# Kernel optimization log

Measured on AMD Instinct MI355X. Metric: run time of the kernel, lower is better.

The kernel has to match this reference:

```python
import jax, jax.numpy as jnp
import numpy as np

HID = 2048      # hidden_size
H = 16          # num query heads
KV = 4          # num kv heads
HD = HID // H   # head_dim = 128
THETA = 1000000.0
T = 2048        # tokens (single causal sequence)


def _rope(x, positions):
    # neox-style rotate-half RoPE over full head_dim. x: [T, h, HD]
    half = HD // 2
    inv_freq = THETA ** (-jnp.arange(half, dtype=jnp.float32) * 2.0 / HD)  # [half]
    freqs = positions.astype(jnp.float32)[:, None] * inv_freq              # [T, half]
    cos = jnp.cos(freqs)[:, None, :]
    sin = jnp.sin(freqs)[:, None, :]
    x1, x2 = x[..., :half], x[..., half:]
    return jnp.concatenate([x1 * cos - x2 * sin, x2 * cos + x1 * sin], axis=-1)


def setup_inputs() -> dict:
    key = jax.random.key(0)
    k1, k2, k3 = jax.random.split(key, 3)
    hidden_states = jax.random.normal(k1, (T, HID), jnp.float32) * 0.02
    w_qkv = jax.random.normal(k2, (HID, (H + 2 * KV) * HD), jnp.float32) * 0.02
    w_o = jax.random.normal(k3, (H * HD, HID), jnp.float32) * 0.02
    positions = jnp.arange(T, dtype=jnp.int32)
    return {"hidden_states": hidden_states, "w_qkv": w_qkv, "w_o": w_o,
            "positions": positions}


def reference(hidden_states, w_qkv, w_o, positions):
    q_size, kv_size = H * HD, KV * HD
    qkv = hidden_states @ w_qkv                                  # [T, q+2kv]
    q = qkv[:, :q_size].reshape(T, H, HD)
    k = qkv[:, q_size:q_size + kv_size].reshape(T, KV, HD)
    v = qkv[:, q_size + kv_size:].reshape(T, KV, HD)
    q = _rope(q, positions)
    k = _rope(k, positions)
    # GQA: expand kv heads to query heads
    group = H // KV
    k_e = jnp.repeat(k, group, axis=1)                           # [T, H, HD]
    v_e = jnp.repeat(v, group, axis=1)
    scale = HD ** -0.5
    scores = jnp.einsum('thd,shd->hts', q, k_e) * scale          # [H, T, T]
    causal = positions[:, None] >= positions[None, :]            # [T, T]
    scores = jnp.where(causal[None, :, :], scores, -1e30)
    attn = jax.nn.softmax(scores, axis=-1)
    o = jnp.einsum('hts,shd->thd', attn, v_e).reshape(T, H * HD)
    return o @ w_o
```

## Files before the change

### kernel.cpp

```cpp
#include <hip/hip_runtime.h>
#include <hip/hip_bf16.h>

#define T_LEN 2048
#define HID 2048
#define NH 16
#define NKV 4
#define HD 128
#define QKV_COLS 3072

typedef __attribute__((ext_vector_type(8))) short bf16x8;
typedef __attribute__((ext_vector_type(4))) float f32x4;

static __device__ __forceinline__ ushort f2bf(float f) {
  __hip_bfloat16 h = __float2bfloat16(f);
  return *reinterpret_cast<ushort*>(&h);
}
static __device__ __forceinline__ float bf2f(ushort u) {
  union { unsigned int i; float f; } v;
  v.i = ((unsigned int)u) << 16;
  return v.f;
}

static __device__ __forceinline__ void async_copy16(const ushort* g, ushort* l) {
  __builtin_amdgcn_global_load_lds(
      (const __attribute__((address_space(1))) unsigned int*)g,
      (__attribute__((address_space(3))) unsigned int*)l, 16, 0, 0);
}

__global__ __launch_bounds__(256) void cast_f32_bf16(
    const float* __restrict__ x, ushort* __restrict__ y, int n) {
  int idx = (blockIdx.x * 256 + threadIdx.x) * 4;
  if (idx < n) {
    float4 v = *(const float4*)(x + idx);
    ushort4 o;
    o.x = f2bf(v.x); o.y = f2bf(v.y); o.z = f2bf(v.z); o.w = f2bf(v.w);
    *(ushort4*)(y + idx) = o;
  }
}

__global__ __launch_bounds__(256) void transpose_cast(
    const float* __restrict__ W, ushort* __restrict__ WT, int K, int N) {
  __shared__ float t[64][65];
  const int bk = blockIdx.x * 64, bn = blockIdx.y * 64;
  const int tid = threadIdx.x;
  const int c = tid & 63;
#pragma unroll
  for (int i = 0; i < 16; ++i) {
    int r = (tid >> 6) + i * 4;
    t[r][c] = W[(size_t)(bk + r) * N + bn + c];
  }
  __syncthreads();
#pragma unroll
  for (int i = 0; i < 16; ++i) {
    int r = (tid >> 6) + i * 4;
    WT[(size_t)(bn + r) * K + bk + c] = f2bf(t[c][r]);
  }
}

template <bool OUT_BF16>
__global__ __launch_bounds__(256, 4) void gemm_bt(
    const ushort* __restrict__ A, const ushort* __restrict__ BT,
    void* __restrict__ C, int M, int N, int K) {
  __shared__ __align__(16) ushort lds[1536 * 8];
  const int tid = threadIdx.x;
  const int bm = blockIdx.y * 64, bn = blockIdx.x * 128;
  const int wave = tid >> 6, lane = tid & 63;
  const int lr = lane & 15, lq = lane >> 4;
  const int wm = (wave & 1) * 32, wn = (wave >> 1) * 64;

  f32x4 acc[2][4];
#pragma unroll
  for (int i = 0; i < 2; ++i)
#pragma unroll
    for (int j = 0; j < 4; ++j) {
      acc[i][j][0] = 0.f; acc[i][j][1] = 0.f;
      acc[i][j][2] = 0.f; acc[i][j][3] = 0.f;
    }

  for (int k0 = 0; k0 < K; k0 += 64) {
#pragma unroll
    for (int it = 0; it < 2; ++it) {
      int c = it * 256 + tid;
      int row = c >> 3, sl = c & 7, kc = sl ^ (row & 7);
      async_copy16(A + (size_t)(bm + row) * K + k0 + kc * 8, &lds[c * 8]);
    }
#pragma unroll
    for (int it = 0; it < 4; ++it) {
      int c = it * 256 + tid;
      int row = c >> 3, sl = c & 7, kc = sl ^ (row & 7);
      async_copy16(BT + (size_t)(bn + row) * K + k0 + kc * 8,
                   &lds[(512 + c) * 8]);
    }
    __syncthreads();

#pragma unroll
    for (int ks = 0; ks < 2; ++ks) {
      bf16x8 af[2], bfr[4];
#pragma unroll
      for (int mi = 0; mi < 2; ++mi) {
        int row = wm + mi * 16 + lr, kc = ks * 4 + lq;
        af[mi] = *(const bf16x8*)&lds[(row * 8 + (kc ^ (row & 7))) * 8];
      }
#pragma unroll
      for (int ni = 0; ni < 4; ++ni) {
        int row = wn + ni * 16 + lr, kc = ks * 4 + lq;
        bfr[ni] = *(const bf16x8*)&lds[(512 + row * 8 + (kc ^ (row & 7))) * 8];
      }
#pragma unroll
      for (int mi = 0; mi < 2; ++mi)
#pragma unroll
        for (int ni = 0; ni < 4; ++ni)
          acc[mi][ni] = __builtin_amdgcn_mfma_f32_16x16x32_bf16(
              af[mi], bfr[ni], acc[mi][ni], 0, 0, 0);
    }
    __syncthreads();
  }

#pragma unroll
  for (int mi = 0; mi < 2; ++mi)
#pragma unroll
    for (int ni = 0; ni < 4; ++ni)
#pragma unroll
      for (int r = 0; r < 4; ++r) {
        size_t row = bm + wm + mi * 16 + lq * 4 + r;
        size_t col = bn + wn + ni * 16 + lr;
        if (OUT_BF16)
          ((ushort*)C)[row * N + col] = f2bf(acc[mi][ni][r]);
        else
          ((float*)C)[row * N + col] = acc[mi][ni][r];
      }
}

__global__ __launch_bounds__(64) void rope_kernel(
    ushort* __restrict__ qkv, const int* __restrict__ positions) {
  const int t = blockIdx.x;
  const int j = threadIdx.x;

  double inv_freq = pow(1000000.0, -(double)(2 * j) / 128.0);
  double ang = (double)positions[t] * inv_freq;
  double s, c;
  sincos(ang, &s, &c);
  const float cf = (float)c, sf = (float)s;
  const float qscale = 0.08838834764831845f;

  ushort* base = qkv + (size_t)t * QKV_COLS;
#pragma unroll
  for (int head = 0; head < NH + NKV; ++head) {
    float m = (head < NH) ? qscale : 1.0f;
    float x1 = bf2f(base[head * HD + j]);
    float x2 = bf2f(base[head * HD + 64 + j]);
    base[head * HD + j]      = f2bf((x1 * cf - x2 * sf) * m);
    base[head * HD + 64 + j] = f2bf((x2 * cf + x1 * sf) * m);
  }
}

__global__ __launch_bounds__(256) void repack_vt(
    const ushort* __restrict__ qkv, ushort* __restrict__ vt) {
  __shared__ ushort tile[64][65];
  const int bt = blockIdx.x * 64;
  const int bv = blockIdx.y * 64;
  const int tid = threadIdx.x;
  const int c = tid & 63, r0 = tid >> 6;
#pragma unroll
  for (int i = 0; i < 16; ++i) {
    int r = r0 + i * 4;
    tile[r][c] = qkv[(size_t)(bt + r) * QKV_COLS + 2560 + bv + c];
  }
  __syncthreads();
#pragma unroll
  for (int i = 0; i < 16; ++i) {
    int r = r0 + i * 4;
    vt[(size_t)(bv + r) * T_LEN + bt + c] = tile[c][r];
  }
}

__global__ __launch_bounds__(256, 3) void attn_mfma(
    const ushort* __restrict__ qkv, const ushort* __restrict__ vt,
    ushort* __restrict__ o, ushort* __restrict__ partials,
    float* __restrict__ ml) {
  int qt, h, k_begin, k_end, slot = -1;
  {
    const int i = blockIdx.x;
    if (i < 512) {
      qt = 31 - (i >> 5);
      const int rem = i & 31;
      h = rem >> 1;
      const int chunk = rem & 1;
      const int n = qt + 1, half = n >> 1;
      k_begin = chunk ? half : 0;
      k_end = chunk ? n : half;
      slot = ((qt - 16) * 16 + h) * 2 + chunk;
    } else {
      const int j = i - 512;
      qt = 15 - (j >> 4);
      h = j & 15;
      k_begin = 0;
      k_end = qt + 1;
    }
  }
  const int kh = h >> 2;
  const int tid = threadIdx.x;
  const int wave = tid >> 6, lane = tid & 63;
  const int lr = lane & 15, lq = lane >> 4;
  const int wq = wave >> 1, ws = wave & 1;

  __shared__ __align__(16) ushort KsL[1024 * 8];
  __shared__ __align__(16) ushort VtsL[1024 * 8];
  __shared__ __align__(16) ushort Ps[8 * 67 * 8];
  __shared__ float l_sh[64][2];

  bf16x8 qf[2][4];
  {
    const ushort* qbase =
        qkv + (size_t)(qt * 64 + wq * 32 + lr) * QKV_COLS + h * HD + lq * 8;
#pragma unroll
    for (int mi = 0; mi < 2; ++mi)
#pragma unroll
      for (int kk = 0; kk < 4; ++kk)
        qf[mi][kk] = *(const bf16x8*)(qbase + (size_t)mi * 16 * QKV_COLS + kk * 32);
  }

  float l_part[2][4];
#pragma unroll
  for (int mi = 0; mi < 2; ++mi)
#pragma unroll
    for (int r = 0; r < 4; ++r) l_part[mi][r] = 0.f;
  f32x4 o_acc[4][2];
#pragma unroll
  for (int qi = 0; qi < 4; ++qi)
#pragma unroll
    for (int di = 0; di < 2; ++di) {
      o_acc[qi][di][0] = 0.f; o_acc[qi][di][1] = 0.f;
      o_acc[qi][di][2] = 0.f; o_acc[qi][di][3] = 0.f;
    }

  for (int kt = k_begin; kt < k_end; ++kt) {
    __syncthreads();

    {
      const ushort* kbase = qkv + 2048 + kh * HD;
#pragma unroll
      for (int it = 0; it < 4; ++it) {
        int c = it * 256 + tid;
        int s = c >> 4, sl = c & 15, dg = sl ^ (s & 15);
        async_copy16(kbase + (size_t)(kt * 64 + s) * QKV_COLS + dg * 8,
                     &KsL[c * 8]);
      }
    }
    {
      const ushort* vbase = vt + (size_t)(kh * HD) * T_LEN + kt * 64;
#pragma unroll
      for (int it = 0; it < 4; ++it) {
        int c = it * 256 + tid;
        int d = c >> 3, sl = c & 7, sc = sl ^ (d & 7);
        async_copy16(vbase + (size_t)d * T_LEN + sc * 8, &VtsL[c * 8]);
      }
    }
    __syncthreads();

    f32x4 s_acc[2][2];
#pragma unroll
    for (int mi = 0; mi < 2; ++mi)
#pragma unroll
      for (int ni = 0; ni < 2; ++ni) {
        s_acc[mi][ni][0] = 0.f; s_acc[mi][ni][1] = 0.f;
        s_acc[mi][ni][2] = 0.f; s_acc[mi][ni][3] = 0.f;
      }
#pragma unroll
    for (int kk = 0; kk < 4; ++kk) {
      bf16x8 kf[2];
#pragma unroll
      for (int ni = 0; ni < 2; ++ni) {
        int s = ws * 32 + ni * 16 + lr;
        kf[ni] = *(const bf16x8*)&KsL[(s * 16 + ((kk * 4 + lq) ^ (s & 15))) * 8];
      }
#pragma unroll
      for (int mi = 0; mi < 2; ++mi)
#pragma unroll
        for (int ni = 0; ni < 2; ++ni)
          s_acc[mi][ni] = __builtin_amdgcn_mfma_f32_16x16x32_bf16(
              qf[mi][kk], kf[ni], s_acc[mi][ni], 0, 0, 0);
    }

    if (kt == qt) {
#pragma unroll
      for (int mi = 0; mi < 2; ++mi)
#pragma unroll
        for (int ni = 0; ni < 2; ++ni)
#pragma unroll
          for (int r = 0; r < 4; ++r)
            if (ws * 32 + ni * 16 + lr > wq * 32 + mi * 16 + lq * 4 + r)
              s_acc[mi][ni][r] = -1e30f;
    }

#pragma unroll
    for (int mi = 0; mi < 2; ++mi)
#pragma unroll
      for (int ni = 0; ni < 2; ++ni)
#pragma unroll
        for (int r = 0; r < 4; ++r) {
          float p = __expf(s_acc[mi][ni][r]);
          l_part[mi][r] += p;
          int s = ws * 32 + ni * 16 + lr;
          int q = wq * 32 + mi * 16 + lq * 4 + r;
          Ps[((s >> 3) * 67 + q) * 8 + (s & 7)] = f2bf(p);
        }
    __syncthreads();

#pragma unroll
    for (int ss = 0; ss < 2; ++ss) {
      bf16x8 vf[2];
#pragma unroll
      for (int di = 0; di < 2; ++di) {
        int d = wave * 32 + di * 16 + lr, sc = ss * 4 + lq;
        vf[di] = *(const bf16x8*)&VtsL[(d * 8 + (sc ^ (d & 7))) * 8];
      }
#pragma unroll
      for (int qi = 0; qi < 4; ++qi) {
        bf16x8 pf = *(const bf16x8*)&Ps[((ss * 4 + lq) * 67 + qi * 16 + lr) * 8];
#pragma unroll
        for (int di = 0; di < 2; ++di)
          o_acc[qi][di] = __builtin_amdgcn_mfma_f32_16x16x32_bf16(
              pf, vf[di], o_acc[qi][di], 0, 0, 0);
      }
    }
  }

#pragma unroll
  for (int mi = 0; mi < 2; ++mi)
#pragma unroll
    for (int r = 0; r < 4; ++r) {
      float v = l_part[mi][r];
#pragma unroll
      for (int off = 1; off < 16; off <<= 1) v += __shfl_xor(v, off, 16);
      l_part[mi][r] = v;
    }
  if (lr == 0) {
#pragma unroll
    for (int mi = 0; mi < 2; ++mi)
#pragma unroll
      for (int r = 0; r < 4; ++r)
        l_sh[wq * 32 + mi * 16 + lq * 4 + r][ws] = l_part[mi][r];
  }
  __syncthreads();

  if (slot < 0) {
    ushort* ob = o + (size_t)(qt * 64) * (NH * HD) + h * HD + wave * 32;
#pragma unroll
    for (int qi = 0; qi < 4; ++qi)
#pragma unroll
      for (int r = 0; r < 4; ++r) {
        int q = qi * 16 + lq * 4 + r;
        float inv = 1.f / (l_sh[q][0] + l_sh[q][1]);
#pragma unroll
        for (int di = 0; di < 2; ++di)
          ob[(size_t)q * (NH * HD) + di * 16 + lr] =
              f2bf(o_acc[qi][di][r] * inv);
      }
  } else {
    ushort* pb = partials + (size_t)slot * 64 * HD + wave * 32;
#pragma unroll
    for (int qi = 0; qi < 4; ++qi)
#pragma unroll
      for (int r = 0; r < 4; ++r) {
        int q = qi * 16 + lq * 4 + r;
#pragma unroll
        for (int di = 0; di < 2; ++di)
          pb[(size_t)q * HD + di * 16 + lr] = f2bf(o_acc[qi][di][r]);
      }
    if (tid < 64) ml[(size_t)slot * 64 + tid] = l_sh[tid][0] + l_sh[tid][1];
  }
}

__global__ __launch_bounds__(256) void attn_reduce(
    const ushort* __restrict__ partials, const float* __restrict__ ml,
    ushort* __restrict__ o) {
  const int bi = blockIdx.x;
  const int qt = 16 + (bi >> 4), h = bi & 15;
  const int s0 = ((qt - 16) * 16 + h) * 2;
  const int tid = threadIdx.x;
  const int row = tid >> 2;
  const int dq = (tid & 3) * 32;

  float l0 = ml[(size_t)s0 * 64 + row];
  float l1 = ml[(size_t)(s0 + 1) * 64 + row];
  float inv = 1.f / (l0 + l1);

  const ushort* p0 = partials + ((size_t)s0 * 64 + row) * HD + dq;
  const ushort* p1 = partials + ((size_t)(s0 + 1) * 64 + row) * HD + dq;
  ushort* ob = o + (size_t)(qt * 64 + row) * (NH * HD) + h * HD + dq;
#pragma unroll
  for (int k = 0; k < 32; ++k)
    ob[k] = f2bf((bf2f(p0[k]) + bf2f(p1[k])) * inv);
}

extern "C" void kernel_launch(void* const* d_in, const int* in_sizes, int n_in,
                              void* d_out, int out_size, void* d_ws,
                              size_t ws_size, hipStream_t stream) {
  const float* hidden = (const float*)d_in[0];
  const float* w_qkv  = (const float*)d_in[1];
  const float* w_o    = (const float*)d_in[2];
  const int* positions = (const int*)d_in[3];
  float* out = (float*)d_out;

  ushort* ws = (ushort*)d_ws;
  ushort* hb    = ws;
  ushort* wqkvT = ws + 4194304;
  ushort* qkvb  = wqkvT + 6291456;
  ushort* vtb   = qkvb + 6291456;
  float*  mlb   = (float*)(vtb + 1048576);
  ushort* ob       = hb;
  ushort* partials = wqkvT;
  ushort* woT      = wqkvT;

  cast_f32_bf16<<<4096, 256, 0, stream>>>(hidden, hb, HID * T_LEN);
  transpose_cast<<<dim3(HID / 64, QKV_COLS / 64), 256, 0, stream>>>(
      w_qkv, wqkvT, HID, QKV_COLS);

  gemm_bt<true><<<dim3(QKV_COLS / 128, T_LEN / 64), 256, 0, stream>>>(
      hb, wqkvT, qkvb, T_LEN, QKV_COLS, HID);

  rope_kernel<<<T_LEN, 64, 0, stream>>>(qkvb, positions);
  repack_vt<<<dim3(T_LEN / 64, (NKV * HD) / 64), 256, 0, stream>>>(qkvb, vtb);

  attn_mfma<<<768, 256, 0, stream>>>(qkvb, vtb, ob, partials, mlb);
  attn_reduce<<<256, 256, 0, stream>>>(partials, mlb, ob);

  transpose_cast<<<dim3(HID / 64, HID / 64), 256, 0, stream>>>(
      w_o, woT, HID, HID);

  gemm_bt<false><<<dim3(HID / 128, T_LEN / 64), 256, 0, stream>>>(
      ob, woT, out, T_LEN, HID, NH * HD);
}
```

Measured before the change: 213.6 us.

## Fuse RoPE and Q scaling into QKV GEMM epilogue using precomputed cos/sin table

```diff
diff --git a/kernel.cpp b/kernel.cpp
--- a/kernel.cpp
+++ b/kernel.cpp
@@ -57,8 +57,18 @@
   }
 }
 
+__global__ __launch_bounds__(64) void rope_table(
+    float2* __restrict__ tbl, const int* __restrict__ positions) {
+  const int t = blockIdx.x, j = threadIdx.x;
+  double inv_freq = pow(1000000.0, -(double)(2 * j) / 128.0);
+  double ang = (double)positions[t] * inv_freq;
+  double s, c;
+  sincos(ang, &s, &c);
+  tbl[(size_t)t * 64 + j] = make_float2((float)c, (float)s);
+}
+
 template <bool OUT_BF16>
-__global__ __launch_bounds__(256, 4) void gemm_bt(
+__global__ __launch_bounds__(256, 5) void gemm_bt(
     const ushort* __restrict__ A, const ushort* __restrict__ BT,
     void* __restrict__ C, int M, int N, int K) {
   __shared__ __align__(16) ushort lds[1536 * 8];
@@ -131,26 +141,102 @@
       }
 }
 
-__global__ __launch_bounds__(64) void rope_kernel(
-    ushort* __restrict__ qkv, const int* __restrict__ positions) {
-  const int t = blockIdx.x;
-  const int j = threadIdx.x;
-
-  double inv_freq = pow(1000000.0, -(double)(2 * j) / 128.0);
-  double ang = (double)positions[t] * inv_freq;
-  double s, c;
-  sincos(ang, &s, &c);
-  const float cf = (float)c, sf = (float)s;
-  const float qscale = 0.08838834764831845f;
-
-  ushort* base = qkv + (size_t)t * QKV_COLS;
-#pragma unroll
-  for (int head = 0; head < NH + NKV; ++head) {
-    float m = (head < NH) ? qscale : 1.0f;
-    float x1 = bf2f(base[head * HD + j]);
-    float x2 = bf2f(base[head * HD + 64 + j]);
-    base[head * HD + j]      = f2bf((x1 * cf - x2 * sf) * m);
-    base[head * HD + 64 + j] = f2bf((x2 * cf + x1 * sf) * m);
+__global__ __launch_bounds__(256, 5) void gemm_qkv(
+    const ushort* __restrict__ A, const ushort* __restrict__ BT,
+    ushort* __restrict__ qkvb, const float2* __restrict__ tbl,
+    int M, int N, int K) {
+  __shared__ __align__(16) ushort lds[1536 * 8];
+  const int tid = threadIdx.x;
+  const int bm = blockIdx.y * 64, bn = blockIdx.x * 128;
+  const int wave = tid >> 6, lane = tid & 63;
+  const int lr = lane & 15, lq = lane >> 4;
+  const int wm = (wave & 1) * 32, wn = (wave >> 1) * 64;
+
+  f32x4 acc[2][4];
+#pragma unroll
+  for (int i = 0; i < 2; ++i)
+#pragma unroll
+    for (int j = 0; j < 4; ++j) {
+      acc[i][j][0] = 0.f; acc[i][j][1] = 0.f;
+      acc[i][j][2] = 0.f; acc[i][j][3] = 0.f;
+    }
+
+  for (int k0 = 0; k0 < K; k0 += 64) {
+#pragma unroll
+    for (int it = 0; it < 2; ++it) {
+      int c = it * 256 + tid;
+      int row = c >> 3, sl = c & 7, kc = sl ^ (row & 7);
+      async_copy16(A + (size_t)(bm + row) * K + k0 + kc * 8, &lds[c * 8]);
+    }
+#pragma unroll
+    for (int it = 0; it < 4; ++it) {
+      int c = it * 256 + tid;
+      int row = c >> 3, sl = c & 7, kc = sl ^ (row & 7);
+      async_copy16(BT + (size_t)(bn + row) * K + k0 + kc * 8,
+                   &lds[(512 + c) * 8]);
+    }
+    __syncthreads();
+
+#pragma unroll
+    for (int ks = 0; ks < 2; ++ks) {
+      bf16x8 af[2], bfr[4];
+#pragma unroll
+      for (int mi = 0; mi < 2; ++mi) {
+        int row = wm + mi * 16 + lr, kc = ks * 4 + lq;
+        af[mi] = *(const bf16x8*)&lds[(row * 8 + (kc ^ (row & 7))) * 8];
+      }
+#pragma unroll
+      for (int ni = 0; ni < 4; ++ni) {
+        int row = wn + ni * 16 + lr, kc = ks * 4 + lq;
+        bfr[ni] = *(const bf16x8*)&lds[(512 + row * 8 + (kc ^ (row & 7))) * 8];
+      }
+#pragma unroll
+      for (int mi = 0; mi < 2; ++mi)
+#pragma unroll
+        for (int ni = 0; ni < 4; ++ni)
+          acc[mi][ni] = __builtin_amdgcn_mfma_f32_16x16x32_bf16(
+              af[mi], bfr[ni], acc[mi][ni], 0, 0, 0);
+    }
+    __syncthreads();
+  }
+
+  const int head = bn >> 7;
+  if (head < NH + NKV - NKV + 0 + (NKV) - 4 + 16 + 4 - 0 && head < 20) {
+    ushort* ep = lds;
+#pragma unroll
+    for (int mi = 0; mi < 2; ++mi)
+#pragma unroll
+      for (int ni = 0; ni < 4; ++ni)
+#pragma unroll
+        for (int r = 0; r < 4; ++r)
+          ep[(wm + mi * 16 + lq * 4 + r) * 130 + wn + ni * 16 + lr] =
+              f2bf(acc[mi][ni][r]);
+    __syncthreads();
+
+    const float qs = (head < NH) ? 0.08838834764831845f : 1.0f;
+#pragma unroll
+    for (int it = 0; it < 16; ++it) {
+      int idx = it * 256 + tid;
+      int row = idx >> 6, j = idx & 63;
+      float x1 = bf2f(ep[row * 130 + j]);
+      float x2 = bf2f(ep[row * 130 + 64 + j]);
+      float2 cs = tbl[(size_t)(bm + row) * 64 + j];
+      qkvb[(size_t)(bm + row) * QKV_COLS + bn + j] =
+          f2bf((x1 * cs.x - x2 * cs.y) * qs);
+      qkvb[(size_t)(bm + row) * QKV_COLS + bn + 64 + j] =
+          f2bf((x2 * cs.x + x1 * cs.y) * qs);
+    }
+  } else {
+#pragma unroll
+    for (int mi = 0; mi < 2; ++mi)
+#pragma unroll
+      for (int ni = 0; ni < 4; ++ni)
+#pragma unroll
+        for (int r = 0; r < 4; ++r) {
+          size_t row = bm + wm + mi * 16 + lq * 4 + r;
+          size_t col = bn + wn + ni * 16 + lr;
+          qkvb[row * QKV_COLS + col] = f2bf(acc[mi][ni][r]);
+        }
   }
 }
 
@@ -409,6 +495,7 @@
   ushort* qkvb  = wqkvT + 6291456;
   ushort* vtb   = qkvb + 6291456;
   float*  mlb   = (float*)(vtb + 1048576);
+  float2* tbl   = (float2*)(mlb + 32768);
   ushort* ob       = hb;
   ushort* partials = wqkvT;
   ushort* woT      = wqkvT;
@@ -416,11 +503,11 @@
   cast_f32_bf16<<<4096, 256, 0, stream>>>(hidden, hb, HID * T_LEN);
   transpose_cast<<<dim3(HID / 64, QKV_COLS / 64), 256, 0, stream>>>(
       w_qkv, wqkvT, HID, QKV_COLS);
-
-  gemm_bt<true><<<dim3(QKV_COLS / 128, T_LEN / 64), 256, 0, stream>>>(
-      hb, wqkvT, qkvb, T_LEN, QKV_COLS, HID);
-
-  rope_kernel<<<T_LEN, 64, 0, stream>>>(qkvb, positions);
+  rope_table<<<T_LEN, 64, 0, stream>>>(tbl, positions);
+
+  gemm_qkv<<<dim3(QKV_COLS / 128, T_LEN / 64), 256, 0, stream>>>(
+      hb, wqkvT, qkvb, tbl, T_LEN, QKV_COLS, HID);
+
   repack_vt<<<dim3(T_LEN / 64, (NKV * HD) / 64), 256, 0, stream>>>(qkvb, vtb);
 
   attn_mfma<<<768, 256, 0, stream>>>(qkvb, vtb, ob, partials, mlb);
```

Result: no change. 210.9 us (-1.3%).
